# Optimization experiments

Measured on AMD Instinct MI355X. Metric: run time of the kernel, lower is better.

The kernel has to match this reference:

```python
import jax, jax.numpy as jnp
import numpy as np

NUM_EXPERTS = 8
HIDDEN = 2048
EXPERT_DIM = 2048  # intermediate_size per shard (tp_size=1)
TOTAL_TOKENS = 32768  # divisible by NUM_EXPERTS


def setup_inputs() -> dict:
    key = jax.random.key(0)
    k1, k2, k3 = jax.random.split(key, 3)
    hidden_states = jax.random.normal(k1, (TOTAL_TOKENS, HIDDEN), dtype=jnp.float32)
    # (E, H, 2*D): gate and up projections concatenated on last dim
    gate_up_proj = jax.random.normal(k2, (NUM_EXPERTS, HIDDEN, 2 * EXPERT_DIM), dtype=jnp.float32) * 0.02
    # (E, D, H)
    down_proj = jax.random.normal(k3, (NUM_EXPERTS, EXPERT_DIM, HIDDEN), dtype=jnp.float32) * 0.02
    return {"hidden_states": hidden_states, "gate_up_proj": gate_up_proj, "down_proj": down_proj}


def reference(hidden_states, gate_up_proj, down_proj):
    E, H = gate_up_proj.shape[0], gate_up_proj.shape[1]
    # tokens are pre-sorted per expert: (E, T, H)
    x = hidden_states.reshape(E, -1, H)
    # grouped GEMM: (E,T,H) @ (E,H,2D) -> (E,T,2D)
    gate_up = jnp.einsum('eth,ehd->etd', x, gate_up_proj)
    gate, up = jnp.split(gate_up, 2, axis=-1)
    # SwiGLU epilogue then down projection: (E,T,D) @ (E,D,H) -> (E,T,H)
    act = up * jax.nn.silu(gate)
    out = jnp.einsum('etd,edh->eth', act, down_proj)
    # tp_size=1 -> all_reduce is identity
    return out.reshape(-1, H)
```

## Files before the change

kernel.cpp:

```cpp
#include <hip/hip_runtime.h>


#define E_EXPERTS 8
#define TPE 4096
#define KD 2048

typedef __bf16 bf16_t;
typedef __bf16 bf16x4 __attribute__((ext_vector_type(4)));
typedef __bf16 bf16x8 __attribute__((ext_vector_type(8)));
typedef float f32x4 __attribute__((ext_vector_type(4)));

#define GLOAD16(src, dst)                                               \
  __builtin_amdgcn_global_load_lds(                                     \
      (const __attribute__((address_space(1))) void*)(src),             \
      (__attribute__((address_space(3))) void*)(dst), 16, 0, 0)

__global__ void cvt_f32_bf16_kernel(const float* __restrict__ in,
                                    bf16_t* __restrict__ out, long n4) {
  long i = (long)blockIdx.x * blockDim.x + threadIdx.x;
  const long stride = (long)gridDim.x * blockDim.x;
  const float4* in4 = (const float4*)in;
  bf16x4* out4 = (bf16x4*)out;
  for (; i < n4; i += stride) {
    float4 v = in4[i];
    bf16x4 o = {(bf16_t)v.x, (bf16_t)v.y, (bf16_t)v.z, (bf16_t)v.w};
    out4[i] = o;
  }
}

__global__ void transpose_cvt_kernel(const float* __restrict__ W,
                                     bf16_t* __restrict__ WT, int K, int N) {
  __shared__ float tile[64][65];
  const int e = blockIdx.z;
  const float* Wp = W + (size_t)e * K * N;
  bf16_t* Tp = WT + (size_t)e * N * K;
  const int n0 = blockIdx.x * 64, k0 = blockIdx.y * 64;
  const int rr = threadIdx.x >> 4;
  const int cc = (threadIdx.x & 15) * 4;
#pragma unroll
  for (int p = 0; p < 4; ++p) {
    const int k = rr + p * 16;
    float4 v = *(const float4*)(Wp + (size_t)(k0 + k) * N + n0 + cc);
    tile[k][cc + 0] = v.x;
    tile[k][cc + 1] = v.y;
    tile[k][cc + 2] = v.z;
    tile[k][cc + 3] = v.w;
  }
  __syncthreads();
#pragma unroll
  for (int p = 0; p < 4; ++p) {
    const int n = rr + p * 16;
    bf16x4 o;
#pragma unroll
    for (int j = 0; j < 4; ++j) o[j] = (bf16_t)tile[cc + j][n];
    *(bf16x4*)(Tp + (size_t)(n0 + n) * K + k0 + cc) = o;
  }
}

#define MMA_H(MP, AF, BF, QN)                                                \
  do {                                                                       \
    _Pragma("unroll") for (int kk = 0; kk < 2; ++kk) {                       \
      _Pragma("unroll") for (int mm = 0; mm < 2; ++mm) {                     \
        _Pragma("unroll") for (int n = 0; n < 2; ++n) {                      \
          acc[(MP)*2 + mm][(QN)*2 + n] =                                     \
              __builtin_amdgcn_mfma_f32_16x16x32_bf16(                       \
                  AF[mm][kk], BF[n][kk], acc[(MP)*2 + mm][(QN)*2 + n], 0, 0, \
                  0);                                                        \
        }                                                                    \
      }                                                                      \
    }                                                                        \
  } while (0)

template <bool FUSED, int NTN>
__global__ __launch_bounds__(512, 2) void moe_gemm8_kernel(
    const bf16_t* __restrict__ A, const bf16_t* __restrict__ Bm,
    void* __restrict__ Cout) {
  constexpr int NT = KD / 64;

  __shared__ alignas(16) bf16_t As[2][256][64];
  __shared__ alignas(16) bf16_t Bs[2][256][64];

  const int NWG = gridDim.x;
  int wg = blockIdx.x;
  wg = (wg & 7) * (NWG >> 3) + (wg >> 3);
  const int e = wg / (16 * NTN);
  const int rem = wg % (16 * NTN);
  const int mt = rem / NTN, ntile = rem % NTN;
  const int t0 = mt * 256, n0 = ntile * 256;

  const int tid = threadIdx.x;
  const int wid = tid >> 6, lane = tid & 63;
  const int wr = wid >> 2, wc = wid & 3;

  const bf16_t* Ae = A + (size_t)e * TPE * KD + (size_t)t0 * KD;
  const bf16_t* Be = Bm + (size_t)e * (size_t)(FUSED ? 4096 : 2048) * KD;

  const int slr = lane >> 3;
  const int sel = ((lane & 7) ^ slr) * 8;

  auto stageA = [&](int kt, int h) {
    const int ktw = kt & (NT - 1);
    const int k0 = ktw * 64;
    const int buf = kt & 1;
#pragma unroll
    for (int i = 0; i < 2; ++i) {
      const int r0 = h * 128 + wid * 16 + i * 8;
      GLOAD16(Ae + (size_t)(r0 + slr) * KD + k0 + sel, &As[buf][r0][0]);
    }
  };
  auto stageB = [&](int kt, int h) {
    const int ktw = kt & (NT - 1);
    const int k0 = ktw * 64;
    const int buf = kt & 1;
#pragma unroll
    for (int i = 0; i < 2; ++i) {
      const int r0 = h * 128 + wid * 16 + i * 8;
      const int R = n0 + r0 + slr;
      int srow;
      if constexpr (FUSED)
        srow = ((R >> 5) << 4) + (R & 15) + ((R >> 4) & 1) * 2048;
      else
        srow = R;
      GLOAD16(Be + (size_t)srow * KD + k0 + sel, &Bs[buf][r0][0]);
    }
  };

  const int la = lane & 15, kg4 = lane >> 4;

  f32x4 acc[8][4] = {};
  bf16x8 afP[2][2], afQ[2][2];
  bf16x8 bA[2][2], bB[2][2];

  auto readAh = [&](int buf, int mp, bf16x8 (&dst)[2][2]) {
#pragma unroll
    for (int mm = 0; mm < 2; ++mm) {
      const int row = wr * 128 + mp * 32 + mm * 16 + la;
#pragma unroll
      for (int kk = 0; kk < 2; ++kk) {
        const int ch = ((kk * 4 + kg4) ^ (la & 7)) * 8;
        dst[mm][kk] = *(const bf16x8*)&As[buf][row][ch];
      }
    }
  };
  auto readBh = [&](int buf, int qn, bf16x8 (&dst)[2][2]) {
#pragma unroll
    for (int n = 0; n < 2; ++n) {
      const int row = wc * 64 + qn * 32 + n * 16 + la;
#pragma unroll
      for (int kk = 0; kk < 2; ++kk) {
        const int ch = ((kk * 4 + kg4) ^ (la & 7)) * 8;
        dst[n][kk] = *(const bf16x8*)&Bs[buf][row][ch];
      }
    }
  };

#define W8 asm volatile("s_waitcnt lgkmcnt(8)" ::: "memory")
#define W4 asm volatile("s_waitcnt lgkmcnt(4)" ::: "memory")
#define W0 asm volatile("s_waitcnt lgkmcnt(0)" ::: "memory")
#define VMC4 asm volatile("s_waitcnt vmcnt(4)" ::: "memory")
#define BAR __builtin_amdgcn_s_barrier()
#define SCHED0 __builtin_amdgcn_sched_barrier(0)
#define PRIO1 __builtin_amdgcn_s_setprio(1)
#define PRIO0 __builtin_amdgcn_s_setprio(0)

#define TILE(kt, buf, BX, BY)                          \
  do {                                                 \
                                               \
    readBh(buf, 1, BY);                                \
    readAh(buf, 1, afQ);                               \
    stageA((kt) + 1, 0);                               \
    W8; SCHED0;                                        \
    PRIO1; MMA_H(0, afP, BX, 0); PRIO0;                \
                                               \
    W4; SCHED0;                                        \
    PRIO1; MMA_H(0, afP, BY, 1); PRIO0;                \
    BAR;                                               \
                                               \
    readAh(buf, 2, afP);                               \
    stageA((kt) + 1, 1);                               \
    W4; SCHED0;                                        \
    PRIO1; MMA_H(1, afQ, BY, 1); PRIO0;                \
                                               \
    PRIO1; MMA_H(1, afQ, BX, 0); PRIO0;                \
    BAR;                                               \
                                               \
    readAh(buf, 3, afQ);                               \
    stageB((kt) + 2, 0);                               \
    W4; SCHED0;                                        \
    PRIO1; MMA_H(2, afP, BX, 0); PRIO0;                \
                                               \
    PRIO1; MMA_H(2, afP, BY, 1); PRIO0;                \
    BAR;                                               \
                                               \
    stageB((kt) + 2, 1);                               \
    W0; SCHED0;                                        \
    PRIO1; MMA_H(3, afQ, BY, 1); PRIO0;                \
                                               \
    VMC4;                                              \
    readAh((buf) ^ 1, 0, afP);                         \
    readBh((buf) ^ 1, 0, BY);                          \
    PRIO1; MMA_H(3, afQ, BX, 0); PRIO0;                \
    BAR;                                               \
  } while (0)

  stageA(0, 0); stageA(0, 1);
  stageB(0, 0); stageB(0, 1);
  stageB(1, 0); stageB(1, 1);
  VMC4;
  BAR;
  readAh(0, 0, afP);
  readBh(0, 0, bA);

  for (int kt = 0; kt < NT; kt += 2) {
    TILE(kt, 0, bA, bB);
    TILE(kt + 1, 1, bB, bA);
  }

  const int lg = lane >> 4;
  const int rbase = t0 + wr * 128;
  if constexpr (FUSED) {
    bf16_t* Cp = (bf16_t*)Cout + (size_t)e * TPE * KD;
    const int jb = (n0 + wc * 64) >> 1;
#pragma unroll
    for (int m = 0; m < 8; ++m)
#pragma unroll
      for (int p = 0; p < 2; ++p)
#pragma unroll
        for (int r = 0; r < 4; ++r) {
          const int row = rbase + m * 16 + lg * 4 + r;
          const int col = jb + p * 16 + la;
          const float g = acc[m][2 * p][r], u = acc[m][2 * p + 1][r];
          const float s = 1.0f / (1.0f + __expf(-g));
          Cp[(size_t)row * KD + col] = (bf16_t)(u * g * s);
        }
  } else {
    float* Cp = (float*)Cout + (size_t)e * TPE * KD;
#pragma unroll
    for (int m = 0; m < 8; ++m)
#pragma unroll
      for (int n = 0; n < 4; ++n)
#pragma unroll
        for (int r = 0; r < 4; ++r) {
          const int row = rbase + m * 16 + lg * 4 + r;
          const int col = n0 + wc * 64 + n * 16 + la;
          Cp[(size_t)row * KD + col] = acc[m][n][r];
        }
  }
#undef W8
#undef W4
#undef W0
#undef VMC4
#undef BAR
#undef SCHED0
#undef PRIO1
#undef PRIO0
}

extern "C" void kernel_launch(void* const* d_in, const int* in_sizes, int n_in,
                              void* d_out, int out_size, void* d_ws,
                              size_t ws_size, hipStream_t stream) {
  const float* hs = (const float*)d_in[0];
  const float* w1 = (const float*)d_in[1];
  const float* w2 = (const float*)d_in[2];

  char* ws = (char*)d_ws;
  bf16_t* xb = (bf16_t*)(ws);
  bf16_t* w1t = (bf16_t*)(ws + (size_t)134217728);
  bf16_t* w2t = (bf16_t*)(ws + (size_t)268435456);
  bf16_t* act = (bf16_t*)(ws + (size_t)335544320);

  const long n4 = (long)E_EXPERTS * TPE * KD / 4;
  cvt_f32_bf16_kernel<<<2048, 256, 0, stream>>>(hs, xb, n4);
  transpose_cvt_kernel<<<dim3(64, 32, 8), 256, 0, stream>>>(w1, w1t, 2048, 4096);
  transpose_cvt_kernel<<<dim3(32, 32, 8), 256, 0, stream>>>(w2, w2t, 2048, 2048);
  moe_gemm8_kernel<true, 16><<<2048, 512, 0, stream>>>(xb, w1t, (void*)act);
  moe_gemm8_kernel<false, 8><<<1024, 512, 0, stream>>>(act, w2t, d_out);
}
```

Baseline: 1.115 ms.

## Shrink MoE GEMM tiles to 128x128 and restructure the MFMA pipeline

Reduces the per-workgroup output tile from 256x256 to 128x128. Each wave now holds a 64x32 accumulator block, LDS buffers are halved, and occupancy is raised to 4 workgroups per CU. The grid grows fourfold and the intra-tile schedule, waitcnt thresholds and fragment reads are rewritten for the smaller tile. The aim is better latency hiding and more workgroups in flight. The cost is lower arithmetic intensity per loaded byte and more global/L2 traffic for A and B.

```diff
diff --git a/kernel.cpp b/kernel.cpp
--- a/kernel.cpp
+++ b/kernel.cpp
@@ -57,36 +57,23 @@
   }
 }
 
-#define MMA_H(MP, AF, BF, QN)                                                \
-  do {                                                                       \
-    _Pragma("unroll") for (int kk = 0; kk < 2; ++kk) {                       \
-      _Pragma("unroll") for (int mm = 0; mm < 2; ++mm) {                     \
-        _Pragma("unroll") for (int n = 0; n < 2; ++n) {                      \
-          acc[(MP)*2 + mm][(QN)*2 + n] =                                     \
-              __builtin_amdgcn_mfma_f32_16x16x32_bf16(                       \
-                  AF[mm][kk], BF[n][kk], acc[(MP)*2 + mm][(QN)*2 + n], 0, 0, \
-                  0);                                                        \
-        }                                                                    \
-      }                                                                      \
-    }                                                                        \
-  } while (0)
-
 template <bool FUSED, int NTN>
-__global__ __launch_bounds__(512, 2) void moe_gemm8_kernel(
+__global__ __launch_bounds__(512, 4) void moe_gemm128_kernel(
     const bf16_t* __restrict__ A, const bf16_t* __restrict__ Bm,
     void* __restrict__ Cout) {
   constexpr int NT = KD / 64;
 
-  __shared__ alignas(16) bf16_t As[2][256][64];
-  __shared__ alignas(16) bf16_t Bs[2][256][64];
+  __shared__ alignas(16) bf16_t As[2][128][64];
+  __shared__ alignas(16) bf16_t Bs[2][128][64];
 
   const int NWG = gridDim.x;
   int wg = blockIdx.x;
   wg = (wg & 7) * (NWG >> 3) + (wg >> 3);
-  const int e = wg / (16 * NTN);
-  const int rem = wg % (16 * NTN);
+  const int per = 32 * NTN;
+  const int e = wg / per;
+  const int rem = wg % per;
   const int mt = rem / NTN, ntile = rem % NTN;
-  const int t0 = mt * 256, n0 = ntile * 256;
+  const int t0 = mt * 128, n0 = ntile * 128;
 
   const int tid = threadIdx.x;
   const int wid = tid >> 6, lane = tid & 63;
@@ -102,39 +89,33 @@
     const int ktw = kt & (NT - 1);
     const int k0 = ktw * 64;
     const int buf = kt & 1;
-#pragma unroll
-    for (int i = 0; i < 2; ++i) {
-      const int r0 = h * 128 + wid * 16 + i * 8;
-      GLOAD16(Ae + (size_t)(r0 + slr) * KD + k0 + sel, &As[buf][r0][0]);
-    }
+    const int r0 = h * 64 + wid * 8;
+    GLOAD16(Ae + (size_t)(r0 + slr) * KD + k0 + sel, &As[buf][r0][0]);
   };
   auto stageB = [&](int kt, int h) {
     const int ktw = kt & (NT - 1);
     const int k0 = ktw * 64;
     const int buf = kt & 1;
-#pragma unroll
-    for (int i = 0; i < 2; ++i) {
-      const int r0 = h * 128 + wid * 16 + i * 8;
-      const int R = n0 + r0 + slr;
-      int srow;
-      if constexpr (FUSED)
-        srow = ((R >> 5) << 4) + (R & 15) + ((R >> 4) & 1) * 2048;
-      else
-        srow = R;
-      GLOAD16(Be + (size_t)srow * KD + k0 + sel, &Bs[buf][r0][0]);
-    }
+    const int r0 = h * 64 + wid * 8;
+    const int R = n0 + r0 + slr;
+    int srow;
+    if constexpr (FUSED)
+      srow = ((R >> 5) << 4) + (R & 15) + ((R >> 4) & 1) * 2048;
+    else
+      srow = R;
+    GLOAD16(Be + (size_t)srow * KD + k0 + sel, &Bs[buf][r0][0]);
   };
 
   const int la = lane & 15, kg4 = lane >> 4;
 
-  f32x4 acc[8][4] = {};
+  f32x4 acc[4][2] = {};
   bf16x8 afP[2][2], afQ[2][2];
-  bf16x8 bA[2][2], bB[2][2];
-
-  auto readAh = [&](int buf, int mp, bf16x8 (&dst)[2][2]) {
+  bf16x8 bX[2], bY[2];
+
+  auto readAm = [&](int buf, int mp, bf16x8 (&dst)[2][2]) {
 #pragma unroll
     for (int mm = 0; mm < 2; ++mm) {
-      const int row = wr * 128 + mp * 32 + mm * 16 + la;
+      const int row = wr * 64 + mp * 32 + mm * 16 + la;
 #pragma unroll
       for (int kk = 0; kk < 2; ++kk) {
         const int ch = ((kk * 4 + kg4) ^ (la & 7)) * 8;
@@ -142,118 +123,114 @@
       }
     }
   };
-  auto readBh = [&](int buf, int qn, bf16x8 (&dst)[2][2]) {
-#pragma unroll
-    for (int n = 0; n < 2; ++n) {
-      const int row = wc * 64 + qn * 32 + n * 16 + la;
-#pragma unroll
-      for (int kk = 0; kk < 2; ++kk) {
-        const int ch = ((kk * 4 + kg4) ^ (la & 7)) * 8;
-        dst[n][kk] = *(const bf16x8*)&Bs[buf][row][ch];
-      }
+  auto readBn = [&](int buf, int nf, bf16x8 (&dst)[2]) {
+    const int row = wc * 32 + nf * 16 + la;
+#pragma unroll
+    for (int kk = 0; kk < 2; ++kk) {
+      const int ch = ((kk * 4 + kg4) ^ (la & 7)) * 8;
+      dst[kk] = *(const bf16x8*)&Bs[buf][row][ch];
     }
   };
 
-#define W8 asm volatile("s_waitcnt lgkmcnt(8)" ::: "memory")
+#define W6 asm volatile("s_waitcnt lgkmcnt(6)" ::: "memory")
 #define W4 asm volatile("s_waitcnt lgkmcnt(4)" ::: "memory")
 #define W0 asm volatile("s_waitcnt lgkmcnt(0)" ::: "memory")
-#define VMC4 asm volatile("s_waitcnt vmcnt(4)" ::: "memory")
+#define VMC2 asm volatile("s_waitcnt vmcnt(2)" ::: "memory")
 #define BAR __builtin_amdgcn_s_barrier()
 #define SCHED0 __builtin_amdgcn_sched_barrier(0)
 #define PRIO1 __builtin_amdgcn_s_setprio(1)
 #define PRIO0 __builtin_amdgcn_s_setprio(0)
 
-#define TILE(kt, buf, BX, BY)                          \
-  do {                                                 \
-                                               \
-    readBh(buf, 1, BY);                                \
-    readAh(buf, 1, afQ);                               \
-    stageA((kt) + 1, 0);                               \
-    W8; SCHED0;                                        \
-    PRIO1; MMA_H(0, afP, BX, 0); PRIO0;                \
-                                               \
-    W4; SCHED0;                                        \
-    PRIO1; MMA_H(0, afP, BY, 1); PRIO0;                \
-    BAR;                                               \
-                                               \
-    readAh(buf, 2, afP);                               \
-    stageA((kt) + 1, 1);                               \
-    W4; SCHED0;                                        \
-    PRIO1; MMA_H(1, afQ, BY, 1); PRIO0;                \
-                                               \
-    PRIO1; MMA_H(1, afQ, BX, 0); PRIO0;                \
-    BAR;                                               \
-                                               \
-    readAh(buf, 3, afQ);                               \
-    stageB((kt) + 2, 0);                               \
-    W4; SCHED0;                                        \
-    PRIO1; MMA_H(2, afP, BX, 0); PRIO0;                \
-                                               \
-    PRIO1; MMA_H(2, afP, BY, 1); PRIO0;                \
-    BAR;                                               \
-                                               \
-    stageB((kt) + 2, 1);                               \
-    W0; SCHED0;                                        \
-    PRIO1; MMA_H(3, afQ, BY, 1); PRIO0;                \
-                                               \
-    VMC4;                                              \
-    readAh((buf) ^ 1, 0, afP);                         \
-    readBh((buf) ^ 1, 0, BY);                          \
-    PRIO1; MMA_H(3, afQ, BX, 0); PRIO0;                \
-    BAR;                                               \
+#define MMA_H(AF, NF, BF)                                                   \
+  do {                                                                      \
+    _Pragma("unroll") for (int kk = 0; kk < 2; ++kk) {                      \
+      _Pragma("unroll") for (int mm = 0; mm < 2; ++mm) {                    \
+        accp[mm][NF] = __builtin_amdgcn_mfma_f32_16x16x32_bf16(             \
+            AF[mm][kk], BF[kk], accp[mm][NF], 0, 0, 0);                     \
+      }                                                                     \
+    }                                                                       \
   } while (0)
+
+#define TILE(kt, buf)                                                       \
+  do {                                                                      \
+    \
+    readAm(buf, 0, afP);                                                    \
+    readBn(buf, 0, bX);                                                     \
+    readBn(buf, 1, bY);                                                     \
+    readAm(buf, 1, afQ);                                                    \
+    stageA((kt) + 1, 0);                                                    \
+    W6; SCHED0;                                                             \
+    { auto& accp = accL;                                                    \
+      PRIO1; MMA_H(afP, 0, bX); PRIO0;                                      \
+                                                                    \
+      stageA((kt) + 1, 1);                                                  \
+      W4; SCHED0;                                                           \
+      PRIO1; MMA_H(afP, 1, bY); PRIO0;                                      \
+      BAR; }                                                                \
+                                                                    \
+    stageB((kt) + 2, 0);                                                    \
+    W0; SCHED0;                                                             \
+    { auto& accp = accH;                                                    \
+      PRIO1; MMA_H(afQ, 1, bY); PRIO0;                                      \
+                                                                    \
+      stageB((kt) + 2, 1);                                                  \
+      PRIO1; MMA_H(afQ, 0, bX); PRIO0; }                                    \
+    VMC2;                                                                   \
+    BAR;                                                                    \
+  } while (0)
+
+  auto accL = (f32x4(*)[2]) & acc[0];
+  auto accH = (f32x4(*)[2]) & acc[2];
 
   stageA(0, 0); stageA(0, 1);
   stageB(0, 0); stageB(0, 1);
   stageB(1, 0); stageB(1, 1);
-  VMC4;
+  VMC2;
   BAR;
-  readAh(0, 0, afP);
-  readBh(0, 0, bA);
 
   for (int kt = 0; kt < NT; kt += 2) {
-    TILE(kt, 0, bA, bB);
-    TILE(kt + 1, 1, bB, bA);
+    TILE(kt, 0);
+    TILE(kt + 1, 1);
   }
 
   const int lg = lane >> 4;
-  const int rbase = t0 + wr * 128;
+  const int rbase = t0 + wr * 64;
   if constexpr (FUSED) {
     bf16_t* Cp = (bf16_t*)Cout + (size_t)e * TPE * KD;
-    const int jb = (n0 + wc * 64) >> 1;
-#pragma unroll
-    for (int m = 0; m < 8; ++m)
-#pragma unroll
-      for (int p = 0; p < 2; ++p)
+    const int jb = (n0 + wc * 32) >> 1;
+#pragma unroll
+    for (int m = 0; m < 4; ++m)
+#pragma unroll
+      for (int r = 0; r < 4; ++r) {
+        const int row = rbase + m * 16 + lg * 4 + r;
+        const int col = jb + la;
+        const float g = acc[m][0][r], u = acc[m][1][r];
+        const float s = 1.0f / (1.0f + __expf(-g));
+        Cp[(size_t)row * KD + col] = (bf16_t)(u * g * s);
+      }
+  } else {
+    float* Cp = (float*)Cout + (size_t)e * TPE * KD;
+#pragma unroll
+    for (int m = 0; m < 4; ++m)
+#pragma unroll
+      for (int n = 0; n < 2; ++n)
 #pragma unroll
         for (int r = 0; r < 4; ++r) {
           const int row = rbase + m * 16 + lg * 4 + r;
-          const int col = jb + p * 16 + la;
-          const float g = acc[m][2 * p][r], u = acc[m][2 * p + 1][r];
-          const float s = 1.0f / (1.0f + __expf(-g));
-          Cp[(size_t)row * KD + col] = (bf16_t)(u * g * s);
-        }
-  } else {
-    float* Cp = (float*)Cout + (size_t)e * TPE * KD;
-#pragma unroll
-    for (int m = 0; m < 8; ++m)
-#pragma unroll
-      for (int n = 0; n < 4; ++n)
-#pragma unroll
-        for (int r = 0; r < 4; ++r) {
-          const int row = rbase + m * 16 + lg * 4 + r;
-          const int col = n0 + wc * 64 + n * 16 + la;
+          const int col = n0 + wc * 32 + n * 16 + la;
           Cp[(size_t)row * KD + col] = acc[m][n][r];
         }
   }
-#undef W8
+#undef W6
 #undef W4
 #undef W0
-#undef VMC4
+#undef VMC2
 #undef BAR
 #undef SCHED0
 #undef PRIO1
 #undef PRIO0
+#undef MMA_H
+#undef TILE
 }
 
 extern "C" void kernel_launch(void* const* d_in, const int* in_sizes, int n_in,
@@ -273,6 +250,6 @@
   cvt_f32_bf16_kernel<<<2048, 256, 0, stream>>>(hs, xb, n4);
   transpose_cvt_kernel<<<dim3(64, 32, 8), 256, 0, stream>>>(w1, w1t, 2048, 4096);
   transpose_cvt_kernel<<<dim3(32, 32, 8), 256, 0, stream>>>(w2, w2t, 2048, 2048);
-  moe_gemm8_kernel<true, 16><<<2048, 512, 0, stream>>>(xb, w1t, (void*)act);
-  moe_gemm8_kernel<false, 8><<<1024, 512, 0, stream>>>(act, w2t, d_out);
-}
+  moe_gemm128_kernel<true, 32><<<8192, 512, 0, stream>>>(xb, w1t, (void*)act);
+  moe_gemm128_kernel<false, 16><<<4096, 512, 0, stream>>>(act, w2t, d_out);
+}
```

New measurement: 1.289 ms. +15.6%, slower.
